# Kernel tuning notes

Measured on AMD Instinct MI355X. Metric: run time of the kernel, lower is better.

The kernel has to match this reference:

```python
import jax, jax.numpy as jnp
import numpy as np

B, N, DIM, H = 16, 197, 768, 12
HD = DIM // H
SCALE = HD ** -0.5
T = 4 * B * N          # uncompressed new-token stream from the 4 frames
M = B * N + T          # cache tokens + new tokens (gather source length)
INNER = 64             # restoration MLP inner dim
FF = 4 * DIM

def _ln(x, g, b, eps=1e-5):
    m = jnp.mean(x, axis=-1, keepdims=True)
    v = jnp.var(x, axis=-1, keepdims=True)
    return (x - m) * jax.lax.rsqrt(v + eps) * g + b

def _quick_gelu(x):
    return x * jax.nn.sigmoid(1.702 * x)

def setup_inputs():
    key = jax.random.key(0)
    ks = jax.random.split(key, 16)
    s = 0.02
    return {
        'list_hidden_states': jax.random.normal(ks[0], (1, T, DIM), jnp.float32),
        'diff_pre_proj': jax.random.normal(ks[1], (4, B, N, DIM), jnp.float32),
        'hqkv_cache': jax.random.normal(ks[2], (4, B, N, DIM), jnp.float32),
        'ln1_g': jnp.ones((DIM,), jnp.float32), 'ln1_b': jnp.zeros((DIM,), jnp.float32),
        'wq': jax.random.normal(ks[3], (DIM, DIM), jnp.float32) * s, 'bq': jnp.zeros((DIM,), jnp.float32),
        'wk': jax.random.normal(ks[4], (DIM, DIM), jnp.float32) * s, 'bk': jnp.zeros((DIM,), jnp.float32),
        'wv': jax.random.normal(ks[5], (DIM, DIM), jnp.float32) * s, 'bv': jnp.zeros((DIM,), jnp.float32),
        'rest_w1': jax.random.normal(ks[6], (DIM, INNER), jnp.float32) * s,
        'rest_w2': jax.random.normal(ks[7], (INNER, 4 * DIM), jnp.float32) * s,
        'wo': jax.random.normal(ks[8], (DIM, DIM), jnp.float32) * s, 'bo': jnp.zeros((DIM,), jnp.float32),
        'ln2_g': jnp.ones((DIM,), jnp.float32), 'ln2_b': jnp.zeros((DIM,), jnp.float32),
        'fc1_w': jax.random.normal(ks[9], (DIM, FF), jnp.float32) * s, 'fc1_b': jnp.zeros((FF,), jnp.float32),
        'fc2_w': jax.random.normal(ks[10], (FF, DIM), jnp.float32) * s, 'fc2_b': jnp.zeros((DIM,), jnp.float32),
        'gather_idxs': jax.random.randint(ks[11], (4, B, N), 0, M),
        'reuse_map': jax.random.bernoulli(ks[12], 0.5, (4, B, N)),
    }

def _forward(list_hidden_states, diff_pre_proj, hqkv_cache,
             ln1_g, ln1_b, wq, bq, wk, bk, wv, bv,
             rest_w1, rest_w2, wo, bo, ln2_g, ln2_b,
             fc1_w, fc1_b, fc2_w, fc2_b, gather_idxs, reuse_map):
    h_cache, q_cache, k_cache, v_cache = hqkv_cache  # each [B,N,DIM]
    hs = list_hidden_states                          # [1,T,DIM]
    # layer_norm1 + QKV projection on the new tokens
    x = _ln(hs, ln1_g, ln1_b)
    q_new = x @ wq + bq
    k_new = x @ wk + bk
    v_new = x @ wv + bv
    # cache concat -> [M, DIM]
    h_p = jnp.concatenate([h_cache.reshape(-1, DIM), hs[0]], 0)
    q_p = jnp.concatenate([q_cache.reshape(-1, DIM), q_new[0]], 0)
    k_p = jnp.concatenate([k_cache.reshape(-1, DIM), k_new[0]], 0)
    v_p = jnp.concatenate([v_cache.reshape(-1, DIM), v_new[0]], 0)
    # index-based gather across the 4 frames -> [4,B,N,DIM]
    h_g = h_p[gather_idxs]
    q_g = q_p[gather_idxs]
    k_g = k_p[gather_idxs]
    v_g = v_p[gather_idxs]
    # restoration MLP on diffs, applied only at reused positions
    diff = jax.nn.gelu(diff_pre_proj @ rest_w1) @ rest_w2   # [4,B,N,4*DIM]
    hd, qd, kd, vd = jnp.split(diff, 4, axis=-1)
    m = reuse_map[..., None]
    h_g = h_g + jnp.where(m, hd, 0.0)
    q_g = q_g + jnp.where(m, qd, 0.0)
    k_g = k_g + jnp.where(m, kd, 0.0)
    v_g = v_g + jnp.where(m, vd, 0.0)
    # manual bmm-softmax-bmm attention over 4*B sequences
    FB = 4 * B
    q = q_g.reshape(FB, N, H, HD) * SCALE
    k = k_g.reshape(FB, N, H, HD)
    v = v_g.reshape(FB, N, H, HD)
    attn = jax.nn.softmax(jnp.einsum('bqhd,bkhd->bhqk', q, k), axis=-1)
    pre_proj = jnp.einsum('bhqk,bkhd->bqhd', attn, v).reshape(4, B, N, DIM)
    h_g = h_g.reshape(4, B, N, DIM)
    # last layer: keep only the CLS token
    h_cls = h_g[:, :, :1]
    pre_cls = pre_proj[:, :, :1]
    out = h_cls + (pre_cls @ wo + bo)
    resid = out
    out = _ln(out, ln2_g, ln2_b)
    out = _quick_gelu(out @ fc1_w + fc1_b) @ fc2_w + fc2_b  # CLIP MLP
    return resid + out   # [4,B,1,DIM]

def reference(list_hidden_states, diff_pre_proj, hqkv_cache,
              ln1_g, ln1_b, wq, bq, wk, bk, wv, bv,
              rest_w1, rest_w2, wo, bo, ln2_g, ln2_b,
              fc1_w, fc1_b, fc2_w, fc2_b, gather_idxs, reuse_map):
    return _forward(list_hidden_states, diff_pre_proj, hqkv_cache,
                    ln1_g, ln1_b, wq, bq, wk, bk, wv, bv,
                    rest_w1, rest_w2, wo, bo, ln2_g, ln2_b,
                    fc1_w, fc1_b, fc2_w, fc2_b, gather_idxs, reuse_map)
```

## Files before the change

kernel.cpp:

```cpp
#include <hip/hip_runtime.h>
#include <hip/hip_bf16.h>

#define TT 12608
#define NC 3152
#define DIM 768
#define NPOS 197
#define NH 12
#define HD 64
#define FB_N 64
#define FF 3072
#define INNER_D 64
#define NCOLS 1536

#define NB_TW  1728
#define NB_TW1 48
#define NB_S1  (NB_TW + NB_TW1 + TT)
#define NB_INN 197
#define NB_QF  6
#define NB_KV  1248
#define NB_S2  (NB_INN + NB_QF + NB_KV)

typedef __bf16 bf16x8 __attribute__((ext_vector_type(8)));
typedef float f32x4 __attribute__((ext_vector_type(4)));

__device__ inline float wred_sum(float v){
  #pragma unroll
  for (int o = 32; o > 0; o >>= 1) v += __shfl_down(v, o, 64);
  return v;
}
__device__ inline float wred_max(float v){
  #pragma unroll
  for (int o = 32; o > 0; o >>= 1) v = fmaxf(v, __shfl_down(v, o, 64));
  return v;
}

__device__ __forceinline__ void gl_lds16(const __bf16* g, __bf16* l) {
  __builtin_amdgcn_global_load_lds(
      (const __attribute__((address_space(1))) void*)g,
      (__attribute__((address_space(3))) void*)l, 16, 0, 0);
}

__global__ void detect_flag_kernel(const int* __restrict__ gidx, const unsigned char* __restrict__ rm,
                                   int* __restrict__ flag, int* __restrict__ det)
{
  int g = blockIdx.x * 256 + threadIdx.x;
  int la = 0, lb = 0;
  if (g < TT) {
    int idx = gidx[g];
    if (idx >= NC) flag[idx - NC] = 1;
    unsigned char v = rm[g];
    if (v) { if (g & 3) la = 1; else lb = 1; }
  }
  unsigned long long ba = __ballot(la != 0), bb = __ballot(lb != 0);
  if ((threadIdx.x & 63) == 0) {
    if (ba) atomicOr(&det[0], 1);
    if (bb) atomicOr(&det[1], 1);
  }
}

__launch_bounds__(1024)
__global__ void scan_kernel(const int* __restrict__ flag, const unsigned char* __restrict__ rm,
                            const int* __restrict__ det, unsigned char* __restrict__ mask,
                            int* __restrict__ rowlist, int* __restrict__ remap,
                            int* __restrict__ mrowlist, int* __restrict__ mremap,
                            int* __restrict__ mc)
{
  __shared__ int wsumA[16], wsumB[16];
  __shared__ int baseA, baseB;
  int t = threadIdx.x, lane = t & 63, wv = t >> 6;
  int mode = (!det[0]) ? 0 : (det[1] ? 1 : 2);
  if (t == 0) { baseA = 0; baseB = 0; }
  __syncthreads();
  for (int start = 0; start < TT; start += 1024) {
    int i = start + t;
    int fA = 0, fB = 0;
    if (i < TT) {
      fA = flag[i];
      unsigned char mb_;
      if (mode == 0)      mb_ = ((const int*)rm)[i] != 0;
      else if (mode == 1) mb_ = rm[i] != 0;
      else                mb_ = ((const float*)rm)[i] != 0.0f;
      mask[i] = mb_;
      fB = mb_;
    }
    unsigned long long mbA = __ballot(fA != 0);
    unsigned long long mbB = __ballot(fB != 0);
    int rankA = __popcll(mbA & ((1ULL << lane) - 1ULL));
    int rankB = __popcll(mbB & ((1ULL << lane) - 1ULL));
    if (lane == 0) { wsumA[wv] = __popcll(mbA); wsumB[wv] = __popcll(mbB); }
    __syncthreads();
    int woffA = 0, woffB = 0;
    for (int w2 = 0; w2 < wv; w2++) { woffA += wsumA[w2]; woffB += wsumB[w2]; }
    if (fA) { int pos = baseA + woffA + rankA; rowlist[pos] = i; remap[i] = pos; }
    if (fB) { int pos = baseB + woffB + rankB; mrowlist[pos] = i; mremap[i] = pos; }
    __syncthreads();
    if (t == 0) {
      int ta = 0, tb = 0;
      for (int w2 = 0; w2 < 16; w2++) { ta += wsumA[w2]; tb += wsumB[w2]; }
      baseA += ta; baseB += tb;
    }
    __syncthreads();
  }
  if (t == 0) { mc[0] = baseA; mc[1] = baseB; }
}

__launch_bounds__(256)
__global__ void stage1_kernel(const float* __restrict__ wk, const float* __restrict__ wvw,
                              const float* __restrict__ wq, const float* __restrict__ w1,
                              const float* __restrict__ hs,
                              const float* __restrict__ ln1g, const float* __restrict__ ln1b,
                              const int* __restrict__ rowlist, const int* __restrict__ mc,
                              __bf16* __restrict__ wcatT, __bf16* __restrict__ wqT,
                              __bf16* __restrict__ w1T, __bf16* __restrict__ xbf)
{
  __shared__ __align__(16) char pool[4352];
  int b = blockIdx.x, t = threadIdx.x;
  if (b < NB_TW) {
    float (*tile)[33] = (float(*)[33])pool;
    int bz = b / 576, rem = b % 576;
    int bx = rem % 24, by = rem / 24;
    int tx = t & 31, ty = t >> 5;
    const float* src = (bz == 0) ? wk : (bz == 1) ? wvw : wq;
    __bf16* dst = (bz == 0) ? wcatT : (bz == 1) ? (wcatT + (size_t)768 * DIM) : wqT;
    #pragma unroll
    for (int i = 0; i < 32; i += 8)
      tile[ty + i][tx] = src[(size_t)(by*32 + ty + i) * DIM + bx*32 + tx];
    __syncthreads();
    #pragma unroll
    for (int i = 0; i < 32; i += 8)
      dst[(size_t)(bx*32 + ty + i) * DIM + by*32 + tx] = (__bf16)tile[tx][ty + i];
    return;
  }
  if (b < NB_TW + NB_TW1) {
    float (*tile)[33] = (float(*)[33])pool;
    int rem = b - NB_TW;
    int bx = rem % 24, by = rem / 24;
    int tx = t & 31, ty = t >> 5;
    #pragma unroll
    for (int i = 0; i < 32; i += 8)
      tile[ty + i][tx] = w1[(size_t)(bx*32 + ty + i) * INNER_D + by*32 + tx];
    __syncthreads();
    #pragma unroll
    for (int i = 0; i < 32; i += 8)
      w1T[(size_t)(by*32 + ty + i) * DIM + bx*32 + tx] = (__bf16)tile[tx][ty + i];
    return;
  }
  int crow = b - NB_TW - NB_TW1;
  if (crow >= mc[0]) return;
  float* red = (float*)pool;
  int row = rowlist[crow];
  const float* x = hs + (size_t)row * DIM;
  float v0 = x[t], v1 = x[t + 256], v2 = x[t + 512];
  float s = wred_sum(v0 + v1 + v2);
  float q = wred_sum(v0*v0 + v1*v1 + v2*v2);
  int wv = t >> 6, ln = t & 63;
  if (ln == 0) { red[wv] = s; red[4 + wv] = q; }
  __syncthreads();
  float mean = (red[0]+red[1]+red[2]+red[3]) * (1.f/DIM);
  float var  = (red[4]+red[5]+red[6]+red[7]) * (1.f/DIM) - mean*mean;
  float rr = rsqrtf(var + 1e-5f);
  #pragma unroll
  for (int j = 0; j < 3; j++) {
    int c = t + j*256;
    float v = (j==0) ? v0 : (j==1) ? v1 : v2;
    xbf[(size_t)crow*DIM + c] = (__bf16)((v - mean) * rr * ln1g[c] + ln1b[c]);
  }
}

__launch_bounds__(256)
__global__ void stage2_kernel(const __bf16* __restrict__ xbf, const __bf16* __restrict__ wcatT,
                              const float* __restrict__ bk, const float* __restrict__ bv,
                              const float* __restrict__ dpp, const __bf16* __restrict__ w1T,
                              const __bf16* __restrict__ wqT,
                              const int* __restrict__ mrowlist, const int* __restrict__ mc,
                              const int* __restrict__ gidx, const int* __restrict__ remap,
                              __bf16* __restrict__ k_newc, __bf16* __restrict__ v_newc,
                              float* __restrict__ inner_c, float* __restrict__ qfresh)
{
  __shared__ __align__(16) char pool[65536];
  int b = blockIdx.x, t = threadIdx.x;
  int lane = t & 63, wid = t >> 6;
  int fr = lane & 15, fg = lane >> 4;

  if (b < NB_INN) {
    int mcnt = mc[1];
    int row0 = b * 64;
    if (row0 >= mcnt) return;
    typedef __bf16 (*tile_t)[40];
    tile_t As = (tile_t)pool;
    tile_t Bs = (tile_t)(pool + 5120);
    int* rlist = (int*)(pool + 10240);
    int wr = wid >> 1, wc = wid & 1;
    if (t < 64) rlist[t] = mrowlist[min(row0 + t, mcnt - 1)];
    __syncthreads();

    int lr = t >> 2, lc = (t & 3) << 3;
    const float* aG = dpp + (size_t)rlist[lr] * DIM + lc;
    const __bf16* bG = w1T + (size_t)lr * DIM + lc;

    f32x4 acc[2][2];
    #pragma unroll
    for (int m = 0; m < 2; m++)
      #pragma unroll
      for (int n = 0; n < 2; n++) acc[m][n] = (f32x4){0.f, 0.f, 0.f, 0.f};

    for (int k0 = 0; k0 < DIM; k0 += 32) {
      float4 a0 = *(const float4*)(aG + k0);
      float4 a1 = *(const float4*)(aG + k0 + 4);
      bf16x8 av;
      av[0] = (__bf16)a0.x; av[1] = (__bf16)a0.y; av[2] = (__bf16)a0.z; av[3] = (__bf16)a0.w;
      av[4] = (__bf16)a1.x; av[5] = (__bf16)a1.y; av[6] = (__bf16)a1.z; av[7] = (__bf16)a1.w;
      *(bf16x8*)&As[lr][lc] = av;
      *(bf16x8*)&Bs[lr][lc] = *(const bf16x8*)(bG + k0);
      __syncthreads();
      bf16x8 af[2], bb[2];
      #pragma unroll
      for (int m = 0; m < 2; m++) af[m] = *(const bf16x8*)&As[wr*32 + m*16 + fr][fg << 3];
      #pragma unroll
      for (int n = 0; n < 2; n++) bb[n] = *(const bf16x8*)&Bs[wc*32 + n*16 + fr][fg << 3];
      #pragma unroll
      for (int m = 0; m < 2; m++)
        #pragma unroll
        for (int n = 0; n < 2; n++)
          acc[m][n] = __builtin_amdgcn_mfma_f32_16x16x32_bf16(af[m], bb[n], acc[m][n], 0, 0, 0);
      __syncthreads();
    }

    #pragma unroll
    for (int m = 0; m < 2; m++) {
      #pragma unroll
      for (int n = 0; n < 2; n++) {
        int col = wc*32 + n*16 + fr;
        int orow = row0 + wr*32 + m*16 + fg*4;
        #pragma unroll
        for (int r = 0; r < 4; r++) {
          int rr = orow + r;
          if (rr < mcnt) {
            float x = acc[m][n][r];
            float u = 0.7978845608028654f * (x + 0.044715f * x * x * x);
            inner_c[(size_t)rr*INNER_D + col] = 0.5f * x * (1.0f + tanhf(u));
          }
        }
      }
    }
    return;
  }

  if (b < NB_INN + NB_QF) {
    int col0 = (b - NB_INN) * 128;
    typedef __bf16 (*tA_t)[40];
    tA_t As = (tA_t)pool;
    tA_t Bs = (tA_t)(pool + 5632);
    int* rl = (int*)(pool + 16384);
    int wr = wid >> 1, wc = wid & 1;
    if (t < FB_N) {
      int idx = gidx[t * NPOS];
      rl[t] = (idx >= NC) ? remap[idx - NC] : -1;
    }
    __syncthreads();

    f32x4 acc[2][4];
    #pragma unroll
    for (int m = 0; m < 2; m++)
      #pragma unroll
      for (int n = 0; n < 4; n++) acc[m][n] = (f32x4){0.f, 0.f, 0.f, 0.f};

    int ar = t >> 2, ac8 = (t & 3) << 3;
    int crow = rl[ar];
    for (int k0 = 0; k0 < DIM; k0 += 32) {
      bf16x8 av = {};
      if (crow >= 0) av = *(const bf16x8*)(xbf + (size_t)crow*DIM + k0 + ac8);
      *(bf16x8*)&As[ar][ac8] = av;
      #pragma unroll
      for (int q = 0; q < 2; q++) {
        int ch = t*2 + q;
        int brw = ch >> 2, bc8 = (ch & 3) << 3;
        *(bf16x8*)&Bs[brw][bc8] = *(const bf16x8*)(wqT + (size_t)(col0 + brw)*DIM + k0 + bc8);
      }
      __syncthreads();
      bf16x8 af[2], bb[4];
      #pragma unroll
      for (int m = 0; m < 2; m++) af[m] = *(const bf16x8*)&As[wr*32 + m*16 + fr][fg << 3];
      #pragma unroll
      for (int n = 0; n < 4; n++) bb[n] = *(const bf16x8*)&Bs[wc*64 + n*16 + fr][fg << 3];
      #pragma unroll
      for (int m = 0; m < 2; m++)
        #pragma unroll
        for (int n = 0; n < 4; n++)
          acc[m][n] = __builtin_amdgcn_mfma_f32_16x16x32_bf16(af[m], bb[n], acc[m][n], 0, 0, 0);
      __syncthreads();
    }
    #pragma unroll
    for (int m = 0; m < 2; m++) {
      #pragma unroll
      for (int n = 0; n < 4; n++) {
        int col = col0 + wc*64 + n*16 + fr;
        int row = wr*32 + m*16 + fg*4;
        #pragma unroll
        for (int r = 0; r < 4; r++)
          qfresh[(size_t)(row + r)*DIM + col] = acc[m][n][r];
      }
    }
    return;
  }

  {
    int Mc = mc[0];
    int npanels = (Mc + 127) >> 7;
    int b2 = b - NB_INN - NB_QF;
    int xcd = b2 & 7, s2 = b2 >> 3;
    int panel = (s2 / 12) * 8 + xcd;
    if (panel >= npanels) return;
    int col0 = (s2 % 12) * 128;
    int row0 = panel * 128;
    char* poolA0 = pool;
    char* poolA1 = pool + 16384;
    char* poolB0 = pool + 32768;
    char* poolB1 = pool + 49152;
    int wr = wid >> 1, wc = wid & 1;

    int tr = t >> 3;
    int tc = (t & 7) << 4;
    int cbp = tc ^ ((tr & 7) << 4);
    const __bf16* aP[4];
    const __bf16* bP[4];
    #pragma unroll
    for (int c2 = 0; c2 < 4; c2++) {
      int r = c2*32 + tr;
      aP[c2] = xbf + (size_t)min(row0 + r, Mc - 1) * DIM + (cbp >> 1);
      bP[c2] = wcatT + (size_t)(col0 + r) * DIM + (cbp >> 1);
    }

    int rA[4], rB[4];
    #pragma unroll
    for (int m = 0; m < 4; m++) { rA[m] = wr*64 + m*16 + fr; rB[m] = wc*64 + m*16 + fr; }
    int swzf = (fr & 7) << 4;

    f32x4 acc[4][4];
    #pragma unroll
    for (int m = 0; m < 4; m++)
      #pragma unroll
      for (int n = 0; n < 4; n++) acc[m][n] = (f32x4){0.f, 0.f, 0.f, 0.f};

    auto STAGE = [&](int s, char* dA, char* dB) {
      int k0 = s * 64;
      #pragma unroll
      for (int c2 = 0; c2 < 4; c2++) {
        gl_lds16(aP[c2] + k0, (__bf16*)(dA + c2*4096 + t*16));
        gl_lds16(bP[c2] + k0, (__bf16*)(dB + c2*4096 + t*16));
      }
    };

    STAGE(0, poolA0, poolB0);
    for (int s = 0; s < 12; s++) {
      char* curA = (s & 1) ? poolA1 : poolA0;
      char* curB = (s & 1) ? poolB1 : poolB0;
      if (s < 11) {
        STAGE(s + 1, (s & 1) ? poolA0 : poolA1, (s & 1) ? poolB0 : poolB1);
        asm volatile("s_waitcnt vmcnt(8)" ::: "memory");
      } else {
        asm volatile("s_waitcnt vmcnt(0)" ::: "memory");
      }
      __builtin_amdgcn_s_barrier();
      __builtin_amdgcn_sched_barrier(0);
      #pragma unroll
      for (int kk = 0; kk < 2; kk++) {
        int co = (kk*64 + (fg << 4)) ^ swzf;
        bf16x8 af[4], bb[4];
        #pragma unroll
        for (int m = 0; m < 4; m++) af[m] = *(const bf16x8*)(curA + rA[m]*128 + co);
        #pragma unroll
        for (int n = 0; n < 4; n++) bb[n] = *(const bf16x8*)(curB + rB[n]*128 + co);
        #pragma unroll
        for (int m = 0; m < 4; m++)
          #pragma unroll
          for (int n = 0; n < 4; n++)
            acc[m][n] = __builtin_amdgcn_mfma_f32_16x16x32_bf16(af[m], bb[n], acc[m][n], 0, 0, 0);
      }
      __builtin_amdgcn_sched_barrier(0);
      __builtin_amdgcn_s_barrier();
    }

    bool isK = (col0 < 768);
    const float* bias = isK ? bk : bv;
    __bf16* dst = isK ? k_newc : v_newc;
    int cbase = isK ? col0 : col0 - 768;
    __bf16* Ct = (__bf16*)pool;
    #pragma unroll
    for (int h = 0; h < 2; h++) {
      __syncthreads();
      if (wr == h) {
        #pragma unroll
        for (int n = 0; n < 4; n++) {
          int col = wc*64 + n*16 + fr;
          float bc = bias[cbase + col];
          #pragma unroll
          for (int m = 0; m < 4; m++) {
            int rl2 = m*16 + fg*4;
            #pragma unroll
            for (int r = 0; r < 4; r++)
              Ct[(rl2 + r)*128 + col] = (__bf16)(acc[m][n][r] + bc);
          }
        }
      }
      __syncthreads();
      #pragma unroll
      for (int c2 = 0; c2 < 4; c2++) {
        int o = c2*4096 + t*16;
        int rl2 = o >> 8;
        int cb = o & 255;
        int grow = row0 + h*64 + rl2;
        if (grow < Mc)
          *(uint4*)(dst + (size_t)grow*DIM + cbase + (cb >> 1)) = *(const uint4*)((char*)Ct + o);
      }
    }
  }
}

__launch_bounds__(256)
__global__ void cls_gather_kernel(const float* __restrict__ hs, const float* __restrict__ hqkv,
                                  const float* __restrict__ bq,
                                  const float* __restrict__ w2, const float* __restrict__ inner_c,
                                  const int* __restrict__ gidx, const unsigned char* __restrict__ mask,
                                  const int* __restrict__ mremap,
                                  float* __restrict__ h_cls, float* __restrict__ qbase)
{
  int fb = blockIdx.x, t = threadIdx.x;
  int g0 = fb * NPOS;
  int idx = gidx[g0];
  int m = mask[g0];
  const float* q_cache = hqkv + (size_t)NC * DIM;
  __shared__ float inn[INNER_D];
  if (t < INNER_D) inn[t] = m ? inner_c[(size_t)mremap[g0]*INNER_D + t] : 0.f;
  __syncthreads();
  bool fresh = idx >= NC;
  for (int c = t; c < DIM; c += 256) {
    float hv = fresh ? hs[(size_t)(idx - NC)*DIM + c] : hqkv[(size_t)idx*DIM + c];
    float qb = fresh ? bq[c] : q_cache[(size_t)idx*DIM + c];
    if (m) {
      float hd = 0.f, qd = 0.f;
      #pragma unroll 8
      for (int j = 0; j < INNER_D; j++) {
        float iv = inn[j];
        hd += iv * w2[(size_t)j*FF + c];
        qd += iv * w2[(size_t)j*FF + DIM + c];
      }
      hv += hd; qb += qd;
    }
    h_cls[(size_t)fb*DIM + c] = hv;
    qbase[(size_t)fb*DIM + c] = qb;
  }
}

__launch_bounds__(256)
__global__ void pgemm_kernel(const float* __restrict__ X, const float* __restrict__ W,
                             float* __restrict__ part, int N, int K, int kChunk)
{
  int t = threadIdx.x;
  int c = t & 63;
  int rq = t >> 6;
  int col0 = blockIdx.x * 64;
  int k0base = blockIdx.y * kChunk;
  __shared__ __align__(16) float Xs[64][68];
  float acc[16];
  #pragma unroll
  for (int i = 0; i < 16; i++) acc[i] = 0.f;
  for (int k0 = k0base; k0 < k0base + kChunk; k0 += 64) {
    #pragma unroll
    for (int j = 0; j < 4; j++) {
      int v = t + 256*j;
      int rr = v >> 4, cc = (v & 15) << 2;
      *(float4*)&Xs[rr][cc] = *(const float4*)&X[(size_t)rr*K + k0 + cc];
    }
    __syncthreads();
    const float* Wp = W + (size_t)k0*N + col0 + c;
    #pragma unroll 4
    for (int kk = 0; kk < 64; kk += 4) {
      float w0 = Wp[(size_t)(kk+0)*N];
      float w1 = Wp[(size_t)(kk+1)*N];
      float w2 = Wp[(size_t)(kk+2)*N];
      float w3 = Wp[(size_t)(kk+3)*N];
      #pragma unroll
      for (int r = 0; r < 16; r++) {
        float4 xv = *(const float4*)&Xs[rq*16 + r][kk];
        acc[r] += xv.x*w0 + xv.y*w1 + xv.z*w2 + xv.w*w3;
      }
    }
    __syncthreads();
  }
  #pragma unroll
  for (int r = 0; r < 16; r++)
    part[((size_t)blockIdx.y*64 + rq*16 + r)*N + col0 + c] = acc[r];
}

__launch_bounds__(512)
__global__ void attn_cls_kernel(const float* __restrict__ hqkv, const __bf16* __restrict__ k_newc,
                                const __bf16* __restrict__ v_newc, const float* __restrict__ w2,
                                const float* __restrict__ inner_c, const int* __restrict__ gidx,
                                const unsigned char* __restrict__ mask, const int* __restrict__ remap,
                                const int* __restrict__ mremap,
                                const float* __restrict__ qbase, const float* __restrict__ qfresh,
                                float* __restrict__ pre_cls)
{
  int bid = blockIdx.x;
  int fb = bid / NH, h = bid % NH;
  int t = threadIdx.x;
  int lane = t & 63, wv = t >> 6;
  const float* k_cache = hqkv + (size_t)2 * NC * DIM;
  const float* v_cache = hqkv + (size_t)3 * NC * DIM;
  __shared__ float q0[HD], w2q[INNER_D], tj[INNER_D];
  __shared__ float p[200];
  __shared__ int sidx[200];
  __shared__ int smg[200];
  __shared__ float red[16];
  __shared__ float pacc[8][64];
  if (t < HD) {
    size_t qoff = (size_t)fb*DIM + h*HD + t;
    q0[t] = (qbase[qoff] + qfresh[qoff]) * 0.125f;
  }
  int tt = t - 64;
  if (tt >= 0 && tt < NPOS) {
    int g = fb * NPOS + tt;
    int idx = gidx[g];
    if (idx >= NC) idx = NC + remap[idx - NC];
    sidx[tt] = idx;
    smg[tt] = mask[g] ? mremap[g] : -1;
  }
  __syncthreads();
  {
    int j = t >> 3, dg = t & 7;
    const float* wr = w2 + (size_t)j*FF + 2*DIM + h*HD + dg*8;
    float4 a = *(const float4*)wr, b = *(const float4*)(wr + 4);
    const float* q = &q0[dg*8];
    float s = a.x*q[0] + a.y*q[1] + a.z*q[2] + a.w*q[3]
            + b.x*q[4] + b.y*q[5] + b.z*q[6] + b.w*q[7];
    s += __shfl_xor(s, 1); s += __shfl_xor(s, 2); s += __shfl_xor(s, 4);
    if (dg == 0) w2q[j] = s;
  }
  __syncthreads();
  #pragma unroll
  for (int it = 0; it < 4; it++) {
    int n = it*64 + wv*8 + (lane >> 3);
    int dg = lane & 7;
    if (n < NPOS) {
      int idx = sidx[n], mg = smg[n];
      const float* q = &q0[dg*8];
      float s = 0.f;
      if (idx >= NC) {
        bf16x8 kv = *(const bf16x8*)(k_newc + (size_t)(idx - NC)*DIM + h*HD + dg*8);
        #pragma unroll
        for (int j = 0; j < 8; j++) s += q[j] * (float)kv[j];
      } else {
        const float* kr = k_cache + (size_t)idx*DIM + h*HD + dg*8;
        float4 a = *(const float4*)kr, b = *(const float4*)(kr + 4);
        s = a.x*q[0] + a.y*q[1] + a.z*q[2] + a.w*q[3]
          + b.x*q[4] + b.y*q[5] + b.z*q[6] + b.w*q[7];
      }
      if (mg >= 0) {
        const float* ir = inner_c + (size_t)mg*INNER_D + dg*8;
        float4 a = *(const float4*)ir, b = *(const float4*)(ir + 4);
        const float* wq8 = &w2q[dg*8];
        s += a.x*wq8[0] + a.y*wq8[1] + a.z*wq8[2] + a.w*wq8[3]
           + b.x*wq8[4] + b.y*wq8[5] + b.z*wq8[6] + b.w*wq8[7];
      }
      s += __shfl_xor(s, 1); s += __shfl_xor(s, 2); s += __shfl_xor(s, 4);
      if (dg == 0) p[n] = s;
    }
  }
  __syncthreads();
  float lm = (t < NPOS) ? p[t] : -1e30f;
  lm = wred_max(lm);
  if (lane == 0) red[wv] = lm;
  __syncthreads();
  float mx = red[0];
  #pragma unroll
  for (int w = 1; w < 8; w++) mx = fmaxf(mx, red[w]);
  float lp = 0.f;
  if (t < NPOS) { lp = __expf(p[t] - mx); p[t] = lp; }
  float ls = wred_sum(lp);
  if (lane == 0) red[8 + wv] = ls;
  __syncthreads();
  float inv = red[8];
  #pragma unroll
  for (int w = 1; w < 8; w++) inv += red[8 + w];
  inv = 1.0f / inv;
  float tp = 0.f;
  for (int n = wv; n < NPOS; n += 8) {
    int mg = smg[n];
    if (mg >= 0) tp += p[n] * inner_c[(size_t)mg*INNER_D + lane];
  }
  pacc[wv][lane] = tp;
  __syncthreads();
  if (t < INNER_D) tj[t] = pacc[0][t] + pacc[1][t] + pacc[2][t] + pacc[3][t]
                         + pacc[4][t] + pacc[5][t] + pacc[6][t] + pacc[7][t];
  __syncthreads();
  float va = 0.f;
  for (int n = wv; n < NPOS; n += 8) {
    float pn = p[n];
    int idx = sidx[n];
    float vvv;
    if (idx >= NC) vvv = (float)v_newc[(size_t)(idx - NC)*DIM + h*HD + lane];
    else           vvv = v_cache[(size_t)idx*DIM + h*HD + lane];
    va += pn * vvv;
  }
  __syncthreads();
  pacc[wv][lane] = va;
  __syncthreads();
  if (t < HD) {
    float o = pacc[0][t] + pacc[1][t] + pacc[2][t] + pacc[3][t]
            + pacc[4][t] + pacc[5][t] + pacc[6][t] + pacc[7][t];
    const float* wv2 = w2 + 3*DIM + h*HD + t;
    float dd = 0.f;
    for (int j = 0; j < INNER_D; j++) dd += tj[j] * wv2[(size_t)j*FF];
    pre_cls[(size_t)fb*DIM + h*HD + t] = (o + dd) * inv;
  }
}

__launch_bounds__(256)
__global__ void reduce_wo_ln_kernel(const float* __restrict__ partW, const float* __restrict__ bo,
                                    const float* __restrict__ h_cls, const float* __restrict__ g,
                                    const float* __restrict__ b, float* __restrict__ out0,
                                    float* __restrict__ yln)
{
  int row = blockIdx.x, t = threadIdx.x;
  float v[3];
  #pragma unroll
  for (int j = 0; j < 3; j++) {
    int c = t + j*256;
    float s = h_cls[(size_t)row*DIM + c] + bo[c];
    #pragma unroll
    for (int ks = 0; ks < 12; ks++) s += partW[((size_t)ks*FB_N + row)*DIM + c];
    v[j] = s;
    out0[(size_t)row*DIM + c] = s;
  }
  float sm = wred_sum(v[0] + v[1] + v[2]);
  float sq = wred_sum(v[0]*v[0] + v[1]*v[1] + v[2]*v[2]);
  __shared__ float red[8];
  int wv = t >> 6, ln = t & 63;
  if (ln == 0) { red[wv] = sm; red[4 + wv] = sq; }
  __syncthreads();
  float mean = (red[0]+red[1]+red[2]+red[3]) * (1.f/DIM);
  float var  = (red[4]+red[5]+red[6]+red[7]) * (1.f/DIM) - mean*mean;
  float rr = rsqrtf(var + 1e-5f);
  #pragma unroll
  for (int j = 0; j < 3; j++) {
    int c = t + j*256;
    yln[(size_t)row*DIM + c] = (v[j] - mean) * rr * g[c] + b[c];
  }
}

__global__ void reduce_gelu_kernel(const float* __restrict__ partF1, const float* __restrict__ b1,
                                   float* __restrict__ t1)
{
  int i = blockIdx.x * 256 + threadIdx.x;
  int c = i % FF;
  float v = b1[c];
  #pragma unroll
  for (int s = 0; s < 6; s++) v += partF1[(size_t)s*FB_N*FF + i];
  t1[i] = v / (1.0f + __expf(-1.702f * v));
}

__global__ void final_reduce_kernel(const float* __restrict__ out0, const float* __restrict__ b2,
                                    const float* __restrict__ partF2, float* __restrict__ dout)
{
  int i = blockIdx.x * 256 + threadIdx.x;
  int c = i % DIM;
  float v = out0[i] + b2[c];
  #pragma unroll
  for (int s = 0; s < 24; s++) v += partF2[(size_t)s*FB_N*DIM + i];
  dout[i] = v;
}

extern "C" void kernel_launch(void* const* d_in, const int* in_sizes, int n_in,
                              void* d_out, int out_size, void* d_ws, size_t ws_size,
                              hipStream_t stream)
{
  const float* hs   = (const float*)d_in[0];
  const float* dpp  = (const float*)d_in[1];
  const float* hqkv = (const float*)d_in[2];
  const float* ln1g = (const float*)d_in[3];
  const float* ln1b = (const float*)d_in[4];
  const float* wq   = (const float*)d_in[5];
  const float* bq   = (const float*)d_in[6];
  const float* wk   = (const float*)d_in[7];
  const float* bk   = (const float*)d_in[8];
  const float* wvw  = (const float*)d_in[9];
  const float* bv   = (const float*)d_in[10];
  const float* w1   = (const float*)d_in[11];
  const float* w2   = (const float*)d_in[12];
  const float* wo   = (const float*)d_in[13];
  const float* bo   = (const float*)d_in[14];
  const float* ln2g = (const float*)d_in[15];
  const float* ln2b = (const float*)d_in[16];
  const float* fc1w = (const float*)d_in[17];
  const float* fc1b = (const float*)d_in[18];
  const float* fc2w = (const float*)d_in[19];
  const float* fc2b = (const float*)d_in[20];
  const int*   gidx = (const int*)d_in[21];
  const unsigned char* rmap = (const unsigned char*)d_in[22];
  float* outp = (float*)d_out;

  char* ws = (char*)d_ws;
  size_t off = 0;
  auto alloc = [&](size_t bytes) { void* p = ws + off; off += (bytes + 255) & ~(size_t)255; return p; };
  unsigned char* mask = (unsigned char*)alloc(TT);
  int* flag     = (int*)alloc((size_t)TT * 4);
  int* mc       = (int*)alloc(256);
  int* rowlist  = (int*)alloc((size_t)TT * 4);
  int* remap    = (int*)alloc((size_t)TT * 4);
  int* mrowlist = (int*)alloc((size_t)TT * 4);
  int* mremap   = (int*)alloc((size_t)TT * 4);
  __bf16* xbf    = (__bf16*)alloc((size_t)TT * DIM * 2);
  __bf16* wcatT  = (__bf16*)alloc((size_t)NCOLS * DIM * 2);
  __bf16* wqT    = (__bf16*)alloc((size_t)DIM * DIM * 2);
  __bf16* w1T    = (__bf16*)alloc((size_t)INNER_D * DIM * 2);
  __bf16* k_newc = (__bf16*)alloc((size_t)TT * DIM * 2);
  __bf16* v_newc = (__bf16*)alloc((size_t)TT * DIM * 2);
  float* inner_c = (float*)alloc((size_t)TT * INNER_D * 4);
  float* qfresh  = (float*)alloc((size_t)FB_N * DIM * 4);
  float* h_cls  = (float*)alloc((size_t)FB_N * DIM * 4);
  float* qbase  = (float*)alloc((size_t)FB_N * DIM * 4);
  float* precls = (float*)alloc((size_t)FB_N * DIM * 4);
  float* out0   = (float*)alloc((size_t)FB_N * DIM * 4);
  float* yln    = (float*)alloc((size_t)FB_N * DIM * 4);
  float* t1     = (float*)alloc((size_t)FB_N * FF * 4);
  float* partW  = (float*)alloc((size_t)12 * FB_N * DIM * 4);
  float* partF1 = (float*)alloc((size_t)6  * FB_N * FF  * 4);
  float* partF2 = (float*)alloc((size_t)24 * FB_N * DIM * 4);
  (void)ws_size; (void)in_sizes; (void)n_in; (void)out_size;

  hipMemsetAsync(flag, 0, (size_t)TT * 4 + 256, stream);
  detect_flag_kernel<<<(TT + 255) / 256, 256, 0, stream>>>(gidx, rmap, flag, mc + 2);
  scan_kernel<<<1, 1024, 0, stream>>>(flag, rmap, mc + 2, mask, rowlist, remap,
                                      mrowlist, mremap, mc);
  stage1_kernel<<<NB_S1, 256, 0, stream>>>(wk, wvw, wq, w1, hs, ln1g, ln1b, rowlist, mc,
                                           wcatT, wqT, w1T, xbf);
  stage2_kernel<<<NB_S2, 256, 0, stream>>>(xbf, wcatT, bk, bv, dpp, w1T, wqT, mrowlist, mc,
                                           gidx, remap, k_newc, v_newc, inner_c, qfresh);
  cls_gather_kernel<<<FB_N, 256, 0, stream>>>(hs, hqkv, bq, w2, inner_c, gidx, mask,
                                              mremap, h_cls, qbase);
  attn_cls_kernel<<<FB_N * NH, 512, 0, stream>>>(hqkv, k_newc, v_newc, w2, inner_c, gidx, mask,
                                                 remap, mremap, qbase, qfresh, precls);
  pgemm_kernel<<<dim3(12, 12), 256, 0, stream>>>(precls, wo, partW, DIM, DIM, 64);
  reduce_wo_ln_kernel<<<FB_N, 256, 0, stream>>>(partW, bo, h_cls, ln2g, ln2b, out0, yln);
  pgemm_kernel<<<dim3(48, 6), 256, 0, stream>>>(yln, fc1w, partF1, FF, DIM, 128);
  reduce_gelu_kernel<<<768, 256, 0, stream>>>(partF1, fc1b, t1);
  pgemm_kernel<<<dim3(12, 24), 256, 0, stream>>>(t1, fc2w, partF2, DIM, FF, 128);
  final_reduce_kernel<<<192, 256, 0, stream>>>(out0, fc2b, partF2, outp);
}
```

Before: 177.4 us.

## Fuse tail GEMM and reduction kernels into one cooperative kernel with grid syncs

Replaces the six tail launches (Wo GEMM, reduce+LN, fc1 GEMM, reduce+GELU, fc2 GEMM, final reduce) with one cooperative kernel of 384 blocks that separates the phases with grid-wide syncs. The aim is to remove per-launch overhead and inter-kernel gaps in a tail that does little work per launch. In exchange it pays for grid.sync barriers and fixes the grid size, so some blocks sit idle in phases that use fewer blocks.

```diff
diff --git a/kernel.cpp b/kernel.cpp
--- a/kernel.cpp
+++ b/kernel.cpp
@@ -1,5 +1,8 @@
 #include <hip/hip_runtime.h>
 #include <hip/hip_bf16.h>
+#include <hip/hip_cooperative_groups.h>
+
+namespace cg = cooperative_groups;
 
 #define TT 12608
 #define NC 3152
@@ -19,6 +22,7 @@
 #define NB_QF  6
 #define NB_KV  1248
 #define NB_S2  (NB_INN + NB_QF + NB_KV)
+#define NB_TAIL 384
 
 typedef __bf16 bf16x8 __attribute__((ext_vector_type(8)));
 typedef float f32x4 __attribute__((ext_vector_type(4)));
@@ -450,47 +454,6 @@
     h_cls[(size_t)fb*DIM + c] = hv;
     qbase[(size_t)fb*DIM + c] = qb;
   }
-}
-
-__launch_bounds__(256)
-__global__ void pgemm_kernel(const float* __restrict__ X, const float* __restrict__ W,
-                             float* __restrict__ part, int N, int K, int kChunk)
-{
-  int t = threadIdx.x;
-  int c = t & 63;
-  int rq = t >> 6;
-  int col0 = blockIdx.x * 64;
-  int k0base = blockIdx.y * kChunk;
-  __shared__ __align__(16) float Xs[64][68];
-  float acc[16];
-  #pragma unroll
-  for (int i = 0; i < 16; i++) acc[i] = 0.f;
-  for (int k0 = k0base; k0 < k0base + kChunk; k0 += 64) {
-    #pragma unroll
-    for (int j = 0; j < 4; j++) {
-      int v = t + 256*j;
-      int rr = v >> 4, cc = (v & 15) << 2;
-      *(float4*)&Xs[rr][cc] = *(const float4*)&X[(size_t)rr*K + k0 + cc];
-    }
-    __syncthreads();
-    const float* Wp = W + (size_t)k0*N + col0 + c;
-    #pragma unroll 4
-    for (int kk = 0; kk < 64; kk += 4) {
-      float w0 = Wp[(size_t)(kk+0)*N];
-      float w1 = Wp[(size_t)(kk+1)*N];
-      float w2 = Wp[(size_t)(kk+2)*N];
-      float w3 = Wp[(size_t)(kk+3)*N];
-      #pragma unroll
-      for (int r = 0; r < 16; r++) {
-        float4 xv = *(const float4*)&Xs[rq*16 + r][kk];
-        acc[r] += xv.x*w0 + xv.y*w1 + xv.z*w2 + xv.w*w3;
-      }
-    }
-    __syncthreads();
-  }
-  #pragma unroll
-  for (int r = 0; r < 16; r++)
-    part[((size_t)blockIdx.y*64 + rq*16 + r)*N + col0 + c] = acc[r];
 }
 
 __launch_bounds__(512)
@@ -616,59 +579,119 @@
   }
 }
 
+__device__ void pgemm_dev(const float* __restrict__ X, const float* __restrict__ W,
+                          float* __restrict__ part, int N, int K, int kChunk,
+                          int colb, int kb, float (*Xs)[68], int t)
+{
+  int c = t & 63;
+  int rq = t >> 6;
+  int col0 = colb * 64;
+  int k0base = kb * kChunk;
+  float acc[16];
+  #pragma unroll
+  for (int i = 0; i < 16; i++) acc[i] = 0.f;
+  for (int k0 = k0base; k0 < k0base + kChunk; k0 += 64) {
+    #pragma unroll
+    for (int j = 0; j < 4; j++) {
+      int v = t + 256*j;
+      int rr = v >> 4, cc = (v & 15) << 2;
+      *(float4*)&Xs[rr][cc] = *(const float4*)&X[(size_t)rr*K + k0 + cc];
+    }
+    __syncthreads();
+    const float* Wp = W + (size_t)k0*N + col0 + c;
+    #pragma unroll 4
+    for (int kk = 0; kk < 64; kk += 4) {
+      float w0 = Wp[(size_t)(kk+0)*N];
+      float w1 = Wp[(size_t)(kk+1)*N];
+      float w2 = Wp[(size_t)(kk+2)*N];
+      float w3 = Wp[(size_t)(kk+3)*N];
+      #pragma unroll
+      for (int r = 0; r < 16; r++) {
+        float4 xv = *(const float4*)&Xs[rq*16 + r][kk];
+        acc[r] += xv.x*w0 + xv.y*w1 + xv.z*w2 + xv.w*w3;
+      }
+    }
+    __syncthreads();
+  }
+  #pragma unroll
+  for (int r = 0; r < 16; r++)
+    part[((size_t)kb*64 + rq*16 + r)*N + col0 + c] = acc[r];
+}
+
 __launch_bounds__(256)
-__global__ void reduce_wo_ln_kernel(const float* __restrict__ partW, const float* __restrict__ bo,
-                                    const float* __restrict__ h_cls, const float* __restrict__ g,
-                                    const float* __restrict__ b, float* __restrict__ out0,
-                                    float* __restrict__ yln)
-{
-  int row = blockIdx.x, t = threadIdx.x;
-  float v[3];
-  #pragma unroll
-  for (int j = 0; j < 3; j++) {
-    int c = t + j*256;
-    float s = h_cls[(size_t)row*DIM + c] + bo[c];
-    #pragma unroll
-    for (int ks = 0; ks < 12; ks++) s += partW[((size_t)ks*FB_N + row)*DIM + c];
-    v[j] = s;
-    out0[(size_t)row*DIM + c] = s;
-  }
-  float sm = wred_sum(v[0] + v[1] + v[2]);
-  float sq = wred_sum(v[0]*v[0] + v[1]*v[1] + v[2]*v[2]);
-  __shared__ float red[8];
-  int wv = t >> 6, ln = t & 63;
-  if (ln == 0) { red[wv] = sm; red[4 + wv] = sq; }
-  __syncthreads();
-  float mean = (red[0]+red[1]+red[2]+red[3]) * (1.f/DIM);
-  float var  = (red[4]+red[5]+red[6]+red[7]) * (1.f/DIM) - mean*mean;
-  float rr = rsqrtf(var + 1e-5f);
-  #pragma unroll
-  for (int j = 0; j < 3; j++) {
-    int c = t + j*256;
-    yln[(size_t)row*DIM + c] = (v[j] - mean) * rr * g[c] + b[c];
-  }
-}
-
-__global__ void reduce_gelu_kernel(const float* __restrict__ partF1, const float* __restrict__ b1,
-                                   float* __restrict__ t1)
-{
-  int i = blockIdx.x * 256 + threadIdx.x;
-  int c = i % FF;
-  float v = b1[c];
-  #pragma unroll
-  for (int s = 0; s < 6; s++) v += partF1[(size_t)s*FB_N*FF + i];
-  t1[i] = v / (1.0f + __expf(-1.702f * v));
-}
-
-__global__ void final_reduce_kernel(const float* __restrict__ out0, const float* __restrict__ b2,
-                                    const float* __restrict__ partF2, float* __restrict__ dout)
-{
-  int i = blockIdx.x * 256 + threadIdx.x;
-  int c = i % DIM;
-  float v = out0[i] + b2[c];
-  #pragma unroll
-  for (int s = 0; s < 24; s++) v += partF2[(size_t)s*FB_N*DIM + i];
-  dout[i] = v;
+__global__ void tail_kernel(const float* __restrict__ precls, const float* __restrict__ wo,
+                            const float* __restrict__ bo, const float* __restrict__ h_cls,
+                            const float* __restrict__ g2, const float* __restrict__ b2,
+                            const float* __restrict__ fc1w, const float* __restrict__ fc1b,
+                            const float* __restrict__ fc2w, const float* __restrict__ fc2b,
+                            float* __restrict__ out0, float* __restrict__ yln,
+                            float* __restrict__ t1, float* __restrict__ partW,
+                            float* __restrict__ partF1, float* __restrict__ partF2,
+                            float* __restrict__ dout)
+{
+  cg::grid_group grid = cg::this_grid();
+  __shared__ __align__(16) float Xs[64][68];
+  __shared__ float red2[8];
+  int b = blockIdx.x, t = threadIdx.x;
+
+  if (b < 144) pgemm_dev(precls, wo, partW, DIM, DIM, 64, b % 12, b / 12, Xs, t);
+  __threadfence();
+  grid.sync();
+
+  if (b < FB_N) {
+    int row = b;
+    float v[3];
+    #pragma unroll
+    for (int j = 0; j < 3; j++) {
+      int c = t + j*256;
+      float s = h_cls[(size_t)row*DIM + c] + bo[c];
+      #pragma unroll
+      for (int ks = 0; ks < 12; ks++) s += partW[((size_t)ks*FB_N + row)*DIM + c];
+      v[j] = s;
+      out0[(size_t)row*DIM + c] = s;
+    }
+    float sm = wred_sum(v[0] + v[1] + v[2]);
+    float sq = wred_sum(v[0]*v[0] + v[1]*v[1] + v[2]*v[2]);
+    int wv = t >> 6, ln = t & 63;
+    if (ln == 0) { red2[wv] = sm; red2[4 + wv] = sq; }
+    __syncthreads();
+    float mean = (red2[0]+red2[1]+red2[2]+red2[3]) * (1.f/DIM);
+    float var  = (red2[4]+red2[5]+red2[6]+red2[7]) * (1.f/DIM) - mean*mean;
+    float rr = rsqrtf(var + 1e-5f);
+    #pragma unroll
+    for (int j = 0; j < 3; j++) {
+      int c = t + j*256;
+      yln[(size_t)row*DIM + c] = (v[j] - mean) * rr * g2[c] + b2[c];
+    }
+  }
+  __threadfence();
+  grid.sync();
+
+  if (b < 288) pgemm_dev(yln, fc1w, partF1, FF, DIM, 128, b % 48, b / 48, Xs, t);
+  __threadfence();
+  grid.sync();
+
+  for (int i = b*256 + t; i < FB_N*FF; i += NB_TAIL*256) {
+    int c = i % FF;
+    float v = fc1b[c];
+    #pragma unroll
+    for (int s = 0; s < 6; s++) v += partF1[(size_t)s*FB_N*FF + i];
+    t1[i] = v / (1.0f + __expf(-1.702f * v));
+  }
+  __threadfence();
+  grid.sync();
+
+  if (b < 288) pgemm_dev(t1, fc2w, partF2, DIM, FF, 128, b % 12, b / 12, Xs, t);
+  __threadfence();
+  grid.sync();
+
+  for (int i = b*256 + t; i < FB_N*DIM; i += NB_TAIL*256) {
+    int c = i % DIM;
+    float v = out0[i] + fc2b[c];
+    #pragma unroll
+    for (int s = 0; s < 24; s++) v += partF2[(size_t)s*FB_N*DIM + i];
+    dout[i] = v;
+  }
 }
 
 extern "C" void kernel_launch(void* const* d_in, const int* in_sizes, int n_in,
@@ -741,10 +764,12 @@
                                               mremap, h_cls, qbase);
   attn_cls_kernel<<<FB_N * NH, 512, 0, stream>>>(hqkv, k_newc, v_newc, w2, inner_c, gidx, mask,
                                                  remap, mremap, qbase, qfresh, precls);
-  pgemm_kernel<<<dim3(12, 12), 256, 0, stream>>>(precls, wo, partW, DIM, DIM, 64);
-  reduce_wo_ln_kernel<<<FB_N, 256, 0, stream>>>(partW, bo, h_cls, ln2g, ln2b, out0, yln);
-  pgemm_kernel<<<dim3(48, 6), 256, 0, stream>>>(yln, fc1w, partF1, FF, DIM, 128);
-  reduce_gelu_kernel<<<768, 256, 0, stream>>>(partF1, fc1b, t1);
-  pgemm_kernel<<<dim3(12, 24), 256, 0, stream>>>(t1, fc2w, partF2, DIM, FF, 128);
-  final_reduce_kernel<<<192, 256, 0, stream>>>(out0, fc2b, partF2, outp);
-}
+  void* kargs[] = {
+    (void*)&precls, (void*)&wo, (void*)&bo, (void*)&h_cls, (void*)&ln2g, (void*)&ln2b,
+    (void*)&fc1w, (void*)&fc1b, (void*)&fc2w, (void*)&fc2b,
+    (void*)&out0, (void*)&yln, (void*)&t1, (void*)&partW, (void*)&partF1, (void*)&partF2,
+    (void*)&outp
+  };
+  hipLaunchCooperativeKernel((const void*)tail_kernel, dim3(NB_TAIL), dim3(256),
+                             kargs, 0, stream);
+}
```

Result: slower. 584.7 us (+229.6%).
